# Performance work log

Hardware: AMD Instinct MI355X
Metric: run time of the kernel (lower is better)

## Reference

```python
import jax, jax.numpy as jnp
import numpy as np
import math

LAYER_NUMBER = 2          # coeff for query-key layer scaling
HEAD_DIM = 128
NORM_FACTOR = math.sqrt(HEAD_DIM) * LAYER_NUMBER  # apply_query_key_layer_scaling
COEFF = float(LAYER_NUMBER)
MASK_FILL = -10000.0


def setup_inputs() -> dict:
    key = jax.random.key(0)
    k1, k2, k3, k4 = jax.random.split(key, 4)
    sq, b, nh, hn = 2048, 2, 16, HEAD_DIM
    query_layer = jax.random.normal(k1, (sq, b, nh, hn), dtype=jnp.float32)
    key_layer = jax.random.normal(k2, (sq, b, nh, hn), dtype=jnp.float32)
    value_layer = jax.random.normal(k3, (sq, b, nh, hn), dtype=jnp.float32)
    attention_mask = jax.random.bernoulli(k4, 0.1, (b, 1, sq, sq))
    return {
        "query_layer": query_layer,
        "key_layer": key_layer,
        "value_layer": value_layer,
        "attention_mask": attention_mask,
    }


def reference(query_layer, key_layer, value_layer, attention_mask):
    sq, b, nh, hn = query_layer.shape
    # raw scores: QK^T / norm_factor  -> [b, h, sq, sk]
    scores = jnp.einsum("sbhd,tbhd->bhst", query_layer, key_layer) / NORM_FACTOR
    # MatchedScaleMaskSoftmax: scale by coeff (softmax in fp32), mask-fill, softmax
    x = scores * COEFF
    x = jnp.where(attention_mask, MASK_FILL, x)
    probs = jax.nn.softmax(x, axis=-1)
    # zero out rows where every key is masked
    all_k_masked = jnp.all(attention_mask, axis=-1)  # [b, 1, sq]
    probs = probs * (1.0 - all_k_masked.astype(probs.dtype))[..., None]
    # (dropout p=0.0 -> identity)
    # context: probs @ V -> [sq, b, h, hn] -> [sq, b, hidden]
    ctx = jnp.einsum("bhst,tbhd->sbhd", probs, value_layer)
    return ctx.reshape(sq, b, nh * hn)
```

## Files before the change

### kernel.cpp

```cpp
#include <hip/hip_runtime.h>
#include <math.h>

#define SQ   2048
#define DH   128
#define NKT  32
#define SCALEF  0.08838834764831845f
#define SCALE2  0.12751743f
#define NSHIFT2 (-23.083121f)

typedef __attribute__((ext_vector_type(8))) short bf16x8;
typedef __attribute__((ext_vector_type(4))) float f32x4;

__device__ __forceinline__ unsigned short f2b(float f) {
    unsigned int u = __float_as_uint(f);
    u += 0x7FFFu + ((u >> 16) & 1u);
    return (unsigned short)(u >> 16);
}
__device__ __forceinline__ unsigned int cvtpk(float lo, float hi) {
    unsigned int r;
    asm("v_cvt_pk_bf16_f32 %0, %1, %2" : "=v"(r) : "v"(lo), "v"(hi));
    return r;
}
__device__ __forceinline__ float fexp2(float x) {
    float r;
    asm("v_exp_f32 %0, %1" : "=v"(r) : "v"(x));
    return r;
}

typedef __attribute__((address_space(1))) const unsigned int guint;
typedef __attribute__((address_space(3))) unsigned int luint;
__device__ __forceinline__ void load_lds16(const void* g, void* l) {
    __builtin_amdgcn_global_load_lds((guint*)g, (luint*)l, 16, 0, 0);
}


__global__ __launch_bounds__(256)
void prep_k(const float* __restrict__ K, unsigned short* __restrict__ Kp)
{
    int id   = blockIdx.x * 256 + threadIdx.x;
    int quad = id & 3;
    int key  = (id >> 2) & 63;
    int ks   = (id >> 8) & 3;
    int kt   = (id >> 10) & 31;
    int bh   = id >> 15;
    const float* src = K + (size_t)(kt * 64 + key) * 4096 + bh * DH + ks * 32 + quad * 8;
    float4 f0 = *(const float4*)src;
    float4 f1 = *(const float4*)(src + 4);
    uint4 o;
    o.x = cvtpk(f0.x, f0.y); o.y = cvtpk(f0.z, f0.w);
    o.z = cvtpk(f1.x, f1.y); o.w = cvtpk(f1.z, f1.w);
    *(uint4*)(Kp + (size_t)id * 8) = o;
}

__global__ __launch_bounds__(512)
void prep_v(const float* __restrict__ V, unsigned short* __restrict__ Vp)
{
    int t    = blockIdx.x;
    int kt   = t & 31, bh = t >> 5;
    int quad = threadIdx.x & 3;
    int d    = threadIdx.x >> 2;
    const float* vb = V + (size_t)(kt * 64) * 4096 + bh * DH + d;
    unsigned short* ob = Vp + (size_t)t * 8192;
    #pragma unroll
    for (int ks2 = 0; ks2 < 2; ks2++) {
        float f[8];
        #pragma unroll
        for (int j = 0; j < 8; j++)
            f[j] = vb[(size_t)(ks2 * 32 + quad * 8 + j) * 4096];
        uint4 o;
        o.x = cvtpk(f[0], f[1]); o.y = cvtpk(f[2], f[3]);
        o.z = cvtpk(f[4], f[5]); o.w = cvtpk(f[6], f[7]);
        *(uint4*)(ob + ((size_t)(ks2 * 128 + d) * 4 + quad) * 8) = o;
    }
}

__global__ __launch_bounds__(256)
void prep_m(const int* __restrict__ M, unsigned long long* __restrict__ B)
{
    int wid  = blockIdx.x * 4 + (threadIdx.x >> 6);
    int lane = threadIdx.x & 63;
    const int* src = M + (size_t)wid * SQ + lane;
    unsigned long long* dst = B + (size_t)wid * NKT;
    #pragma unroll
    for (int t = 0; t < NKT; t++) {
        unsigned long long bm = __ballot(src[t * 64] != 0);
        if (lane == 0) dst[t] = bm;
    }
}

#define STAGE(Kl, Vl, ktt) do {                                              \
    const unsigned short* kg_ = KpT + (size_t)(ktt) * 8192;                  \
    const unsigned short* vg_ = VpT + (size_t)(ktt) * 8192;                  \
    _Pragma("unroll") for (int i_ = 0; i_ < 4; i_++) {                       \
        int ch_ = w * 64 + i_ * 256;                                         \
        load_lds16(kg_ + (size_t)(ch_ + lane) * 8, &Kl[ch_ * 8]);            \
    }                                                                        \
    _Pragma("unroll") for (int i_ = 0; i_ < 4; i_++) {                       \
        int ch_ = w * 64 + i_ * 256;                                         \
        load_lds16(vg_ + (size_t)(ch_ + lane) * 8, &Vl[ch_ * 8]);            \
    }                                                                        \
} while (0)

#define LOADMR(mr, ktt) do {                                                 \
    _Pragma("unroll") for (int r_ = 0; r_ < 4; r_++) {                       \
        mr[0][r_] = mb0[r_ * NKT + (ktt)];                                   \
        mr[1][r_] = mb1[r_ * NKT + (ktt)];                                   \
    }                                                                        \
} while (0)

#define COMPUTE(Kl, Vl, mr) do {                                             \
    f32x4 s[2][4];                                                           \
    _Pragma("unroll") for (int blk = 0; blk < 2; blk++)                      \
        _Pragma("unroll") for (int nb = 0; nb < 4; nb++)                     \
            s[blk][nb] = (f32x4){0.f, 0.f, 0.f, 0.f};                        \
    __builtin_amdgcn_s_setprio(1);                                           \
    _Pragma("unroll") for (int nb = 0; nb < 4; nb++) {                       \
        bf16x8 bk[4];                                                        \
        _Pragma("unroll") for (int ks = 0; ks < 4; ks++)                     \
            bk[ks] = *(const bf16x8*)&Kl[ks * 2048 + nb * 512 + c * 32 + quad * 8]; \
        _Pragma("unroll") for (int blk = 0; blk < 2; blk++)                  \
            _Pragma("unroll") for (int ks = 0; ks < 4; ks++)                 \
                s[blk][nb] = __builtin_amdgcn_mfma_f32_16x16x32_bf16(aq[blk][ks], bk[ks], s[blk][nb], 0, 0, 0); \
    }                                                                        \
    __builtin_amdgcn_s_setprio(0);                                           \
    _Pragma("unroll") for (int blk = 0; blk < 2; blk++) {                    \
        _Pragma("unroll") for (int r = 0; r < 4; r++) {                      \
            unsigned long long bits = mr[blk][r];                            \
            unsigned wlo = (unsigned)(bits >> c);                            \
            unsigned whi = (unsigned)(bits >> 32) >> c;                      \
            _Pragma("unroll") for (int nbp = 0; nbp < 2; nbp++) {            \
                unsigned wb = nbp ? whi : wlo;                               \
                float p0 = fexp2(fmaf(s[blk][2 * nbp][r],     SCALE2, NSHIFT2)); \
                float p1 = fexp2(fmaf(s[blk][2 * nbp + 1][r], SCALE2, NSHIFT2)); \
                if (wb & 1u)       p0 = 0.0f;                                \
                if (wb & 0x10000u) p1 = 0.0f;                                \
                l[blk][r] += p0 + p1;                                        \
                unsigned pk = cvtpk(p0, p1);                                 \
                int base = nbp * 1024 + blk * 512 + quad * 128 + r * 32 + (c & 7); \
                Pw[base + ((0 + (c >> 3)) ^ quad) * 8] = (unsigned short)pk; \
                Pw[base + ((2 + (c >> 3)) ^ quad) * 8] = (unsigned short)(pk >> 16); \
            }                                                                \
        }                                                                    \
    }                                                                        \
    bf16x8 ap[2][2];                                                         \
    _Pragma("unroll") for (int blk = 0; blk < 2; blk++)                      \
        _Pragma("unroll") for (int ks2 = 0; ks2 < 2; ks2++)                  \
            ap[blk][ks2] = *(const bf16x8*)&Pw[ks2 * 1024 + blk * 512 + c * 32 + ((quad ^ (c >> 2)) * 8)]; \
    __builtin_amdgcn_s_setprio(1);                                           \
    _Pragma("unroll") for (int nb = 0; nb < 8; nb++) {                       \
        bf16x8 bv0 = *(const bf16x8*)&Vl[nb * 512 + c * 32 + quad * 8];      \
        bf16x8 bv1 = *(const bf16x8*)&Vl[4096 + nb * 512 + c * 32 + quad * 8]; \
        _Pragma("unroll") for (int blk = 0; blk < 2; blk++) {                \
            oa[blk][nb] = __builtin_amdgcn_mfma_f32_16x16x32_bf16(ap[blk][0], bv0, oa[blk][nb], 0, 0, 0); \
            oa[blk][nb] = __builtin_amdgcn_mfma_f32_16x16x32_bf16(ap[blk][1], bv1, oa[blk][nb], 0, 0, 0); \
        }                                                                    \
    }                                                                        \
    __builtin_amdgcn_s_setprio(0);                                           \
} while (0)

#define PIPE_STEP(Kc, Vc, mrC, Kn, Vn, mrN, ktn) do {                        \
    __builtin_amdgcn_s_barrier();                                            \
    STAGE(Kn, Vn, (ktn));                                                    \
    LOADMR(mrN, (ktn));                                                      \
    asm volatile("s_waitcnt vmcnt(16)" ::: "memory");                        \
    __builtin_amdgcn_s_barrier();                                            \
    __builtin_amdgcn_sched_barrier(0);                                       \
    COMPUTE(Kc, Vc, mrC);                                                    \
} while (0)

__global__ __launch_bounds__(256, 2)
void fa2(const float* __restrict__ Q, const unsigned short* __restrict__ Kp,
         const unsigned short* __restrict__ Vp, const unsigned long long* __restrict__ MB,
         float* __restrict__ out)
{
    __shared__ __align__(16) unsigned short K_lds[2][64 * 128];
    __shared__ __align__(16) unsigned short V_lds[2][64 * 128];
    __shared__ __align__(16) unsigned short P_lds[4 * 2048];

    const int tid  = threadIdx.x;
    const int w    = tid >> 6;
    const int lane = tid & 63;
    const int quad = lane >> 4;
    const int c    = lane & 15;

    const int bid0 = blockIdx.x;
    const int bid  = ((bid0 & 7) << 6) | (bid0 >> 3);
    const int qt  = bid & 15;
    const int bh  = bid >> 4;
    const int b_i = bh >> 4;
    const int qbase = qt * 128 + w * 32;
    const size_t bh_off = (size_t)bh * DH;

    bf16x8 aq[2][4];
    #pragma unroll
    for (int blk = 0; blk < 2; blk++) {
        const float* qrow = Q + (size_t)(qbase + blk * 16 + c) * 4096 + bh_off;
        #pragma unroll
        for (int ks = 0; ks < 4; ks++) {
            const int d0 = ks * 32 + quad * 8;
            float4 f0 = *(const float4*)(qrow + d0);
            float4 f1 = *(const float4*)(qrow + d0 + 4);
            uint4 u;
            u.x = cvtpk(f0.x, f0.y); u.y = cvtpk(f0.z, f0.w);
            u.z = cvtpk(f1.x, f1.y); u.w = cvtpk(f1.z, f1.w);
            aq[blk][ks] = *(bf16x8*)&u;
        }
    }

    f32x4 oa[2][8];
    #pragma unroll
    for (int blk = 0; blk < 2; blk++)
        #pragma unroll
        for (int nb = 0; nb < 8; nb++) oa[blk][nb] = (f32x4){0.f, 0.f, 0.f, 0.f};
    float l[2][4];
    #pragma unroll
    for (int blk = 0; blk < 2; blk++)
        #pragma unroll
        for (int r = 0; r < 4; r++) l[blk][r] = 0.0f;

    const unsigned short* KpT = Kp + (size_t)bh * (NKT * 8192);
    const unsigned short* VpT = Vp + (size_t)bh * (NKT * 8192);
    const unsigned long long* mb0 = MB + (size_t)(b_i * SQ + qbase + quad * 4) * NKT;
    const unsigned long long* mb1 = mb0 + 16 * NKT;
    unsigned short* Pw = &P_lds[w * 2048];

    unsigned long long mrA[2][4], mrB[2][4];

    STAGE(K_lds[0], V_lds[0], 0);
    LOADMR(mrA, 0);

    for (int kt = 0; kt < NKT; kt += 2) {
        PIPE_STEP(K_lds[0], V_lds[0], mrA, K_lds[1], V_lds[1], mrB, kt + 1);
        PIPE_STEP(K_lds[1], V_lds[1], mrB, K_lds[0], V_lds[0], mrA, (kt + 2) & 31);
    }
    asm volatile("s_waitcnt vmcnt(0)" ::: "memory");

    #pragma unroll
    for (int blk = 0; blk < 2; blk++) {
        #pragma unroll
        for (int r = 0; r < 4; r++) {
            float t = l[blk][r];
            t += __shfl_xor(t, 1, 64);
            t += __shfl_xor(t, 2, 64);
            t += __shfl_xor(t, 4, 64);
            t += __shfl_xor(t, 8, 64);
            float inv = (t > 0.0f) ? (1.0f / t) : 0.0f;
            float* orow = out + (size_t)(qbase + blk * 16 + quad * 4 + r) * 4096 + bh_off;
            #pragma unroll
            for (int nb = 0; nb < 8; nb++)
                orow[nb * 16 + c] = oa[blk][nb][r] * inv;
        }
    }
}

__global__ __launch_bounds__(256)
void fa_fallback(const float* __restrict__ Q, const float* __restrict__ K,
                 const float* __restrict__ V, const int* __restrict__ mask,
                 float* __restrict__ out)
{
    __shared__ unsigned short K_lds[64 * 136];
    __shared__ unsigned short Vt_lds[128 * 72];
    __shared__ unsigned short P_lds[4 * 16 * 72];
    const int tid = threadIdx.x, w = tid >> 6, lane = tid & 63, quad = lane >> 4, c = lane & 15;
    const int gid = blockIdx.x, qtile = gid & 31, bh = gid >> 5, b_i = bh >> 4;
    const int q0 = qtile * 64 + w * 16;
    const size_t bh_off = (size_t)bh * DH;
    bf16x8 aq[4];
    {
        const float* qrow = Q + (size_t)(q0 + c) * 4096 + bh_off;
        #pragma unroll
        for (int ks = 0; ks < 4; ks++) {
            const int d0 = ks * 32 + quad * 8;
            float4 f0 = *(const float4*)(qrow + d0);
            float4 f1 = *(const float4*)(qrow + d0 + 4);
            bf16x8 a;
            a[0] = (short)f2b(f0.x); a[1] = (short)f2b(f0.y); a[2] = (short)f2b(f0.z); a[3] = (short)f2b(f0.w);
            a[4] = (short)f2b(f1.x); a[5] = (short)f2b(f1.y); a[6] = (short)f2b(f1.z); a[7] = (short)f2b(f1.w);
            aq[ks] = a;
        }
    }
    float m_i[4], l_i[4];
    #pragma unroll
    for (int r = 0; r < 4; r++) { m_i[r] = -INFINITY; l_i[r] = 0.0f; }
    f32x4 o_acc[8];
    #pragma unroll
    for (int nb = 0; nb < 8; nb++) o_acc[nb] = (f32x4){0.f, 0.f, 0.f, 0.f};
    const int srow = tid >> 2, scol = (tid & 3) * 4;
    const int* mbase = mask + (size_t)b_i * SQ * SQ;
    for (int kt = 0; kt < SQ; kt += 64) {
        __syncthreads();
        {
            const float* krow = K + (size_t)(kt + srow) * 4096 + bh_off;
            const float* vrow = V + (size_t)(kt + srow) * 4096 + bh_off;
            #pragma unroll
            for (int j = 0; j < 8; j++) {
                const int d0 = scol + j * 16;
                float4 kf = *(const float4*)(krow + d0);
                unsigned lo = (unsigned)f2b(kf.x) | ((unsigned)f2b(kf.y) << 16);
                unsigned hi = (unsigned)f2b(kf.z) | ((unsigned)f2b(kf.w) << 16);
                *(uint2*)&K_lds[srow * 136 + d0] = make_uint2(lo, hi);
                float4 vf = *(const float4*)(vrow + d0);
                Vt_lds[(d0 + 0) * 72 + srow] = f2b(vf.x);
                Vt_lds[(d0 + 1) * 72 + srow] = f2b(vf.y);
                Vt_lds[(d0 + 2) * 72 + srow] = f2b(vf.z);
                Vt_lds[(d0 + 3) * 72 + srow] = f2b(vf.w);
            }
        }
        __syncthreads();
        f32x4 s[4];
        #pragma unroll
        for (int nb = 0; nb < 4; nb++) s[nb] = (f32x4){0.f, 0.f, 0.f, 0.f};
        #pragma unroll
        for (int nb = 0; nb < 4; nb++)
            #pragma unroll
            for (int ks = 0; ks < 4; ks++) {
                bf16x8 bk = *(const bf16x8*)&K_lds[(nb * 16 + c) * 136 + ks * 32 + quad * 8];
                s[nb] = __builtin_amdgcn_mfma_f32_16x16x32_bf16(aq[ks], bk, s[nb], 0, 0, 0);
            }
        float rowmax[4];
        #pragma unroll
        for (int r = 0; r < 4; r++) rowmax[r] = -INFINITY;
        #pragma unroll
        for (int r = 0; r < 4; r++) {
            const int* mp = mbase + (size_t)(q0 + quad * 4 + r) * SQ + kt + c;
            #pragma unroll
            for (int nb = 0; nb < 4; nb++) {
                float v = s[nb][r] * SCALEF;
                if (mp[nb * 16] != 0) v = -10000.0f;
                s[nb][r] = v;
                rowmax[r] = fmaxf(rowmax[r], v);
            }
        }
        #pragma unroll
        for (int r = 0; r < 4; r++)
            #pragma unroll
            for (int off = 1; off < 16; off <<= 1)
                rowmax[r] = fmaxf(rowmax[r], __shfl_xor(rowmax[r], off, 64));
        float alpha[4], rowsum[4];
        #pragma unroll
        for (int r = 0; r < 4; r++) {
            float mn = fmaxf(m_i[r], rowmax[r]);
            alpha[r] = __expf(m_i[r] - mn);
            m_i[r] = mn;
            rowsum[r] = 0.0f;
        }
        #pragma unroll
        for (int r = 0; r < 4; r++)
            #pragma unroll
            for (int nb = 0; nb < 4; nb++) {
                float p = __expf(s[nb][r] - m_i[r]);
                rowsum[r] += p;
                P_lds[(w * 16 + quad * 4 + r) * 72 + nb * 16 + c] = f2b(p);
            }
        #pragma unroll
        for (int r = 0; r < 4; r++) {
            #pragma unroll
            for (int off = 1; off < 16; off <<= 1)
                rowsum[r] += __shfl_xor(rowsum[r], off, 64);
            l_i[r] = l_i[r] * alpha[r] + rowsum[r];
        }
        #pragma unroll
        for (int nb = 0; nb < 8; nb++)
            #pragma unroll
            for (int r = 0; r < 4; r++) o_acc[nb][r] *= alpha[r];
        bf16x8 ap[2];
        #pragma unroll
        for (int ks = 0; ks < 2; ks++)
            ap[ks] = *(const bf16x8*)&P_lds[(w * 16 + c) * 72 + ks * 32 + quad * 8];
        #pragma unroll
        for (int nb = 0; nb < 8; nb++)
            #pragma unroll
            for (int ks = 0; ks < 2; ks++) {
                bf16x8 bv = *(const bf16x8*)&Vt_lds[(nb * 16 + c) * 72 + ks * 32 + quad * 8];
                o_acc[nb] = __builtin_amdgcn_mfma_f32_16x16x32_bf16(ap[ks], bv, o_acc[nb], 0, 0, 0);
            }
    }
    float inv[4];
    #pragma unroll
    for (int r = 0; r < 4; r++) inv[r] = (m_i[r] > -9999.0f) ? (1.0f / l_i[r]) : 0.0f;
    #pragma unroll
    for (int r = 0; r < 4; r++) {
        float* orow = out + (size_t)(q0 + quad * 4 + r) * 4096 + bh_off;
        #pragma unroll
        for (int nb = 0; nb < 8; nb++) orow[nb * 16 + c] = o_acc[nb][r] * inv[r];
    }
}

extern "C" void kernel_launch(void* const* d_in, const int* in_sizes, int n_in,
                              void* d_out, int out_size, void* d_ws, size_t ws_size,
                              hipStream_t stream) {
    const float* Q    = (const float*)d_in[0];
    const float* K    = (const float*)d_in[1];
    const float* V    = (const float*)d_in[2];
    const int*   mask = (const int*)d_in[3];
    float* out = (float*)d_out;

    const size_t KP_BYTES = (size_t)32 * 32 * 8192 * 2;
    const size_t NEED = 2 * KP_BYTES + (size_t)4096 * NKT * 8;
    if (ws_size < NEED) {
        fa_fallback<<<dim3(1024), dim3(256), 0, stream>>>(Q, K, V, mask, out);
        return;
    }
    unsigned short* Kp = (unsigned short*)d_ws;
    unsigned short* Vp = (unsigned short*)((char*)d_ws + KP_BYTES);
    unsigned long long* MB = (unsigned long long*)((char*)d_ws + 2 * KP_BYTES);

    prep_k<<<dim3(4096), dim3(256), 0, stream>>>(K, Kp);
    prep_v<<<dim3(1024), dim3(512), 0, stream>>>(V, Vp);
    prep_m<<<dim3(1024), dim3(256), 0, stream>>>(mask, MB);
    fa2<<<dim3(512), dim3(256), 0, stream>>>(Q, Kp, Vp, MB, out);
}
```

Baseline: 271.8 us.

## Swizzle K/V bf16 layout to avoid LDS bank conflicts and merge prep kernels

The K and V preprocessing now writes each 8-element chunk into an XOR-swizzled slot, and the attention kernel reads LDS using the matching swizzled offset. This is meant to remove bank conflicts on the MFMA B-operand reads. The three prep kernels are also merged into one launch, with block-index ranges dispatching the K, V and mask work, to save launch overhead. The V prep block size changes from 512 to 256 threads, with a loop over two halves of the head dimension.

```diff
diff --git a/kernel.cpp b/kernel.cpp
--- a/kernel.cpp
+++ b/kernel.cpp
@@ -35,56 +35,63 @@
 
 
 __global__ __launch_bounds__(256)
-void prep_k(const float* __restrict__ K, unsigned short* __restrict__ Kp)
+void prep_all(const float* __restrict__ K, const float* __restrict__ V,
+              const int* __restrict__ M,
+              unsigned short* __restrict__ Kp, unsigned short* __restrict__ Vp,
+              unsigned long long* __restrict__ B)
 {
-    int id   = blockIdx.x * 256 + threadIdx.x;
-    int quad = id & 3;
-    int key  = (id >> 2) & 63;
-    int ks   = (id >> 8) & 3;
-    int kt   = (id >> 10) & 31;
-    int bh   = id >> 15;
-    const float* src = K + (size_t)(kt * 64 + key) * 4096 + bh * DH + ks * 32 + quad * 8;
-    float4 f0 = *(const float4*)src;
-    float4 f1 = *(const float4*)(src + 4);
-    uint4 o;
-    o.x = cvtpk(f0.x, f0.y); o.y = cvtpk(f0.z, f0.w);
-    o.z = cvtpk(f1.x, f1.y); o.w = cvtpk(f1.z, f1.w);
-    *(uint4*)(Kp + (size_t)id * 8) = o;
-}
-
-__global__ __launch_bounds__(512)
-void prep_v(const float* __restrict__ V, unsigned short* __restrict__ Vp)
-{
-    int t    = blockIdx.x;
-    int kt   = t & 31, bh = t >> 5;
-    int quad = threadIdx.x & 3;
-    int d    = threadIdx.x >> 2;
-    const float* vb = V + (size_t)(kt * 64) * 4096 + bh * DH + d;
-    unsigned short* ob = Vp + (size_t)t * 8192;
-    #pragma unroll
-    for (int ks2 = 0; ks2 < 2; ks2++) {
-        float f[8];
-        #pragma unroll
-        for (int j = 0; j < 8; j++)
-            f[j] = vb[(size_t)(ks2 * 32 + quad * 8 + j) * 4096];
+    const int bid = blockIdx.x;
+    const int tid = threadIdx.x;
+    if (bid < 4096) {
+        int id   = bid * 256 + tid;
+        int quad = id & 3;
+        int key  = (id >> 2) & 63;
+        int ks   = (id >> 8) & 3;
+        int kt   = (id >> 10) & 31;
+        int bh   = id >> 15;
+        int qsrc = quad ^ ((key >> 1) & 3);
+        const float* src = K + (size_t)(kt * 64 + key) * 4096 + bh * DH + ks * 32 + qsrc * 8;
+        float4 f0 = *(const float4*)src;
+        float4 f1 = *(const float4*)(src + 4);
         uint4 o;
-        o.x = cvtpk(f[0], f[1]); o.y = cvtpk(f[2], f[3]);
-        o.z = cvtpk(f[4], f[5]); o.w = cvtpk(f[6], f[7]);
-        *(uint4*)(ob + ((size_t)(ks2 * 128 + d) * 4 + quad) * 8) = o;
-    }
-}
-
-__global__ __launch_bounds__(256)
-void prep_m(const int* __restrict__ M, unsigned long long* __restrict__ B)
-{
-    int wid  = blockIdx.x * 4 + (threadIdx.x >> 6);
-    int lane = threadIdx.x & 63;
-    const int* src = M + (size_t)wid * SQ + lane;
-    unsigned long long* dst = B + (size_t)wid * NKT;
-    #pragma unroll
-    for (int t = 0; t < NKT; t++) {
-        unsigned long long bm = __ballot(src[t * 64] != 0);
-        if (lane == 0) dst[t] = bm;
+        o.x = cvtpk(f0.x, f0.y); o.y = cvtpk(f0.z, f0.w);
+        o.z = cvtpk(f1.x, f1.y); o.w = cvtpk(f1.z, f1.w);
+        *(uint4*)(Kp + (size_t)id * 8) = o;
+    } else if (bid < 5120) {
+        int t    = bid - 4096;
+        int kt   = t & 31, bh = t >> 5;
+        int quad = tid & 3;
+        int d2   = tid >> 2;
+        int s    = (d2 >> 1) & 3;
+        int rb   = (quad ^ s) * 8;
+        unsigned short* ob = Vp + (size_t)t * 8192;
+        #pragma unroll
+        for (int ks2 = 0; ks2 < 2; ks2++) {
+            #pragma unroll
+            for (int dhi = 0; dhi < 2; dhi++) {
+                int d = dhi * 64 + d2;
+                const float* vb = V + (size_t)(kt * 64 + ks2 * 32 + rb) * 4096 + bh * DH + d;
+                float f[8];
+                #pragma unroll
+                for (int j = 0; j < 8; j++)
+                    f[j] = vb[(size_t)j * 4096];
+                uint4 o;
+                o.x = cvtpk(f[0], f[1]); o.y = cvtpk(f[2], f[3]);
+                o.z = cvtpk(f[4], f[5]); o.w = cvtpk(f[6], f[7]);
+                *(uint4*)(ob + ((size_t)(ks2 * 128 + d) * 4 + quad) * 8) = o;
+            }
+        }
+    } else {
+        int b2   = bid - 5120;
+        int wid  = b2 * 4 + (tid >> 6);
+        int lane = tid & 63;
+        const int* src = M + (size_t)wid * SQ + lane;
+        unsigned long long* dst = B + (size_t)wid * NKT;
+        #pragma unroll
+        for (int t = 0; t < NKT; t++) {
+            unsigned long long bm = __ballot(src[t * 64] != 0);
+            if (lane == 0) dst[t] = bm;
+        }
     }
 }
 
@@ -117,7 +124,7 @@
     _Pragma("unroll") for (int nb = 0; nb < 4; nb++) {                       \
         bf16x8 bk[4];                                                        \
         _Pragma("unroll") for (int ks = 0; ks < 4; ks++)                     \
-            bk[ks] = *(const bf16x8*)&Kl[ks * 2048 + nb * 512 + c * 32 + quad * 8]; \
+            bk[ks] = *(const bf16x8*)&Kl[ks * 2048 + nb * 512 + c * 32 + swz8]; \
         _Pragma("unroll") for (int blk = 0; blk < 2; blk++)                  \
             _Pragma("unroll") for (int ks = 0; ks < 4; ks++)                 \
                 s[blk][nb] = __builtin_amdgcn_mfma_f32_16x16x32_bf16(aq[blk][ks], bk[ks], s[blk][nb], 0, 0, 0); \
@@ -148,8 +155,8 @@
             ap[blk][ks2] = *(const bf16x8*)&Pw[ks2 * 1024 + blk * 512 + c * 32 + ((quad ^ (c >> 2)) * 8)]; \
     __builtin_amdgcn_s_setprio(1);                                           \
     _Pragma("unroll") for (int nb = 0; nb < 8; nb++) {                       \
-        bf16x8 bv0 = *(const bf16x8*)&Vl[nb * 512 + c * 32 + quad * 8];      \
-        bf16x8 bv1 = *(const bf16x8*)&Vl[4096 + nb * 512 + c * 32 + quad * 8]; \
+        bf16x8 bv0 = *(const bf16x8*)&Vl[nb * 512 + c * 32 + swz8];          \
+        bf16x8 bv1 = *(const bf16x8*)&Vl[4096 + nb * 512 + c * 32 + swz8];   \
         _Pragma("unroll") for (int blk = 0; blk < 2; blk++) {                \
             oa[blk][nb] = __builtin_amdgcn_mfma_f32_16x16x32_bf16(ap[blk][0], bv0, oa[blk][nb], 0, 0, 0); \
             oa[blk][nb] = __builtin_amdgcn_mfma_f32_16x16x32_bf16(ap[blk][1], bv1, oa[blk][nb], 0, 0, 0); \
@@ -182,6 +189,7 @@
     const int lane = tid & 63;
     const int quad = lane >> 4;
     const int c    = lane & 15;
+    const int swz8 = (quad ^ ((c >> 1) & 3)) * 8;
 
     const int bid0 = blockIdx.x;
     const int bid  = ((bid0 & 7) << 6) | (bid0 >> 3);
@@ -405,8 +413,6 @@
     unsigned short* Vp = (unsigned short*)((char*)d_ws + KP_BYTES);
     unsigned long long* MB = (unsigned long long*)((char*)d_ws + 2 * KP_BYTES);
 
-    prep_k<<<dim3(4096), dim3(256), 0, stream>>>(K, Kp);
-    prep_v<<<dim3(1024), dim3(512), 0, stream>>>(V, Vp);
-    prep_m<<<dim3(1024), dim3(256), 0, stream>>>(mask, MB);
+    prep_all<<<dim3(6144), dim3(256), 0, stream>>>(K, V, mask, Kp, Vp, MB);
     fa2<<<dim3(512), dim3(256), 0, stream>>>(Q, Kp, Vp, MB, out);
 }
```

Result: faster. 264.9 us (-2.5%).
